# Kernel tuning notes

Measured on AMD Instinct MI355X. Metric: run time of the kernel, lower is better.

## Reference

```python
import jax, jax.numpy as jnp
import numpy as np

L, H, DK, DV, D, DH, V, S, B = 2, 12, 64, 64, 768, 3072, 32000, 1024, 2


def _layernorm(x):
    # matches custom LayerNorm: mean over last dim, biased std, no eps, no affine
    mu = jnp.mean(x, axis=-1, keepdims=True)
    sigma = jnp.sqrt(jnp.mean(jnp.square(x - mu), axis=-1, keepdims=True))
    return (x - mu) / sigma


def setup_inputs() -> dict:
    key = jax.random.key(0)
    ks = jax.random.split(key, 12)
    n = lambda k, shp: (0.02 * jax.random.normal(k, shp, dtype=jnp.float32))
    return {
        "x": jax.random.randint(ks[0], (B, S), 0, V),
        "ignore": jax.random.randint(ks[1], (B, S), 0, 2).astype(jnp.int32),
        "emb": n(ks[2], (V, D)),
        "pos": n(ks[3], (S, D)),
        "Wq": n(ks[4], (L, H, D, DK)), "bq": jnp.zeros((L, H, DK), jnp.float32),
        "Wk": n(ks[5], (L, H, D, DK)), "bk": jnp.zeros((L, H, DK), jnp.float32),
        "Wv": n(ks[6], (L, H, D, DV)), "bv": jnp.zeros((L, H, DV), jnp.float32),
        "Wo": n(ks[7], (L, H * DV, D)), "bo": jnp.zeros((L, D), jnp.float32),
        "W1": n(ks[8], (L, D, DH)), "b1": jnp.zeros((L, DH), jnp.float32),
        "W2": n(ks[9], (L, DH, D)), "b2": jnp.zeros((L, D), jnp.float32),
        "Wout": n(ks[10], (D, V)), "bout": jnp.zeros((V,), jnp.float32),
    }


def reference(x, ignore, emb, pos, Wq, bq, Wk, bk, Wv, bv, Wo, bo, W1, b1, W2, b2, Wout, bout):
    b, s = x.shape
    ign0 = (ignore == 0)  # True = valid token
    # token emb + position emb zeroed on ignored positions (dropout = eval/identity)
    h = emb[x] + pos[None, :, :] * ign0[:, :, None].astype(emb.dtype)

    # mask[b,i,j]: attend iff j<=i AND (ignore[j]==0 OR i==j)  (diagonal always kept)
    causal = jnp.tril(jnp.ones((s, s), dtype=bool))
    eye = jnp.eye(s, dtype=bool)
    allow = (ign0[:, None, None, :] | eye[None, None, :, :]) & causal[None, None, :, :]  # [b,1,i,j]

    scale = jnp.sqrt(jnp.asarray(DK, h.dtype))
    for l in range(L):
        q = jnp.einsum('bsd,hdk->bhsk', h, Wq[l]) + bq[l][None, :, None, :]
        k = jnp.einsum('bsd,hdk->bhsk', h, Wk[l]) + bk[l][None, :, None, :]
        v = jnp.einsum('bsd,hdv->bhsv', h, Wv[l]) + bv[l][None, :, None, :]
        scores = jnp.einsum('bhik,bhjk->bhij', q, k) / scale
        scores = jnp.where(allow, scores, -jnp.inf)
        p = jax.nn.softmax(scores, axis=-1)
        sa = jnp.einsum('bhij,bhjv->bhiv', p, v)
        sa = sa.transpose(0, 2, 1, 3).reshape(b, s, H * DV)  # concat heads (head-major order matches torch cat)
        attn_out = sa @ Wo[l] + bo[l]
        z = _layernorm(h + attn_out)
        # NOTE: original FeedForwardLayer applies GELU AFTER linear2 (faithful to source)
        f = jax.nn.gelu((z @ W1[l] + b1[l]) @ W2[l] + b2[l], approximate=False)
        h = _layernorm(z + f)
    return h @ Wout + bout
```

## Files before the change

kernel.cpp:

```cpp
#include <hip/hip_runtime.h>
#include <math.h>

static constexpr int L_ = 2, H_ = 12, D_ = 768, DH_ = 3072, V_ = 32000,
                     S_ = 1024, B_ = 2;
static constexpr int M_ = B_ * S_;

typedef __attribute__((ext_vector_type(4))) float f32x4;
typedef __attribute__((ext_vector_type(8))) short s16x8;
typedef __attribute__((ext_vector_type(2))) unsigned int u32x2;
typedef __attribute__((ext_vector_type(4))) unsigned int u32x4;

__device__ __forceinline__ unsigned short f2bf(float f) {
    unsigned u = __builtin_bit_cast(unsigned, f);
    u = (u + 0x7FFFu + ((u >> 16) & 1u)) >> 16;
    return (unsigned short)u;
}
__device__ __forceinline__ unsigned pack2(float a, float b) {
    return (unsigned)f2bf(a) | ((unsigned)f2bf(b) << 16);
}

__device__ __forceinline__ void gld16(const void* g, void* l) {
    __builtin_amdgcn_global_load_lds(
        (const __attribute__((address_space(1))) unsigned int*)g,
        (__attribute__((address_space(3))) unsigned int*)l, 16, 0, 0);
}

__global__ __launch_bounds__(256) void wtr_kernel(
    const float* __restrict__ in, unsigned short* __restrict__ out, int K, int N)
{
    __shared__ unsigned short t[64 * 68];
    const size_t mo = (size_t)blockIdx.z * K * N;
    in  += mo; out += mo;
    const int n0 = blockIdx.x * 64, k0 = blockIdx.y * 64;
    const int tid = threadIdx.x;
    const int kr = tid >> 2, nc = (tid & 3) * 16;
    const float* src = in + (size_t)(k0 + kr) * N + n0 + nc;
    #pragma unroll
    for (int j = 0; j < 4; ++j) {
        const float4 v = *(const float4*)(src + j * 4);
        *(u32x2*)&t[kr * 68 + nc + j * 4] = (u32x2){pack2(v.x, v.y), pack2(v.z, v.w)};
    }
    __syncthreads();
    const int nr = tid >> 2, kc = (tid & 3) * 16;
    unsigned short v16[16];
    #pragma unroll
    for (int j = 0; j < 16; ++j) v16[j] = t[(kc + j) * 68 + nr];
    unsigned short* dst = out + (size_t)(n0 + nr) * K + k0 + kc;
    ((u32x4*)dst)[0] = *(u32x4*)&v16[0];
    ((u32x4*)dst)[1] = *(u32x4*)&v16[8];
}

__global__ __launch_bounds__(256) void wtr3_kernel(
    const float* __restrict__ Wq, const float* __restrict__ Wk,
    const float* __restrict__ Wv, unsigned short* __restrict__ oq,
    unsigned short* __restrict__ ok, unsigned short* __restrict__ ov)
{
    __shared__ unsigned short t[64 * 68];
    const int z = blockIdx.z;
    const int which = z / 24, zz = z - which * 24;
    const float* in = (which == 0) ? Wq : (which == 1) ? Wk : Wv;
    unsigned short* out = (which == 0) ? oq : (which == 1) ? ok : ov;
    const size_t mo = (size_t)zz * D_ * 64;
    in += mo; out += mo;
    const int k0 = blockIdx.y * 64;
    const int tid = threadIdx.x;
    const int kr = tid >> 2, nc = (tid & 3) * 16;
    const float* src = in + (size_t)(k0 + kr) * 64 + nc;
    #pragma unroll
    for (int j = 0; j < 4; ++j) {
        const float4 v = *(const float4*)(src + j * 4);
        *(u32x2*)&t[kr * 68 + nc + j * 4] = (u32x2){pack2(v.x, v.y), pack2(v.z, v.w)};
    }
    __syncthreads();
    const int nr = tid >> 2, kc = (tid & 3) * 16;
    unsigned short v16[16];
    #pragma unroll
    for (int j = 0; j < 16; ++j) v16[j] = t[(kc + j) * 68 + nr];
    unsigned short* dst = out + (size_t)nr * D_ + k0 + kc;
    ((u32x4*)dst)[0] = *(u32x4*)&v16[0];
    ((u32x4*)dst)[1] = *(u32x4*)&v16[8];
}

__device__ __forceinline__ void gemm_bt_body(
    const unsigned short* __restrict__ A, const unsigned short* __restrict__ BT,
    const float* __restrict__ bias, void* __restrict__ Cp,
    int N, int K, int act, int bx, int by)
{
    __shared__ unsigned short AB[16384];
    unsigned short* As = AB;
    unsigned short* Bs = AB + 8192;
    const int tid = threadIdx.x;
    const int l   = tid & 63, wid = tid >> 6;
    const int wr  = wid >> 1, wc = wid & 1;
    const int brow = by * 128, bn = bx * 128;

    f32x4 acc[4][4];
    #pragma unroll
    for (int i = 0; i < 4; ++i)
        #pragma unroll
        for (int j = 0; j < 4; ++j) acc[i][j] = (f32x4)0.f;

    const int arow = tid >> 3;
    const int aq   = (tid & 7) ^ (arow & 7);
    const unsigned short* Abase = A  + (size_t)(brow + arow) * K + aq * 8;
    const unsigned short* Bbase = BT + (size_t)(bn   + arow) * K + aq * 8;

    for (int k0 = 0; k0 < K; k0 += 64) {
        #pragma unroll
        for (int r = 0; r < 4; ++r)
            gld16(Abase + (size_t)r * 32 * K + k0, (char*)As + r * 4096 + wid * 1024);
        #pragma unroll
        for (int r = 0; r < 4; ++r)
            gld16(Bbase + (size_t)r * 32 * K + k0, (char*)Bs + r * 4096 + wid * 1024);
        __syncthreads();

        #pragma unroll
        for (int kk = 0; kk < 2; ++kk) {
            s16x8 af[4], bf[4];
            #pragma unroll
            for (int mf = 0; mf < 4; ++mf) {
                const int row = wr * 64 + mf * 16 + (l & 15);
                const int gg  = (kk * 4 + (l >> 4)) ^ (row & 7);
                af[mf] = *(const s16x8*)((const char*)As + row * 128 + gg * 16);
            }
            #pragma unroll
            for (int nf = 0; nf < 4; ++nf) {
                const int col = wc * 64 + nf * 16 + (l & 15);
                const int gg  = (kk * 4 + (l >> 4)) ^ (col & 7);
                bf[nf] = *(const s16x8*)((const char*)Bs + col * 128 + gg * 16);
            }
            #pragma unroll
            for (int mf = 0; mf < 4; ++mf)
                #pragma unroll
                for (int nf = 0; nf < 4; ++nf)
                    acc[mf][nf] = __builtin_amdgcn_mfma_f32_16x16x32_bf16(
                        af[mf], bf[nf], acc[mf][nf], 0, 0, 0);
        }
        __syncthreads();
    }

    const int lr = l >> 4, lc = l & 15;
    if (act == 3) {
        #pragma unroll
        for (int nf = 0; nf < 4; ++nf) {
            const int c = wc * 64 + nf * 16 + lc;
            const float bb = bias[bn + c];
            #pragma unroll
            for (int mf = 0; mf < 4; ++mf) {
                const int srel = wr * 64 + mf * 16 + lr * 4;
                u32x2 pk;
                pk[0] = pack2(acc[mf][nf][0] + bb, acc[mf][nf][1] + bb);
                pk[1] = pack2(acc[mf][nf][2] + bb, acc[mf][nf][3] + bb);
                const int byo = (c * 256 + srel * 2) ^ ((c & 7) << 4);
                *(u32x2*)((char*)AB + byo) = pk;
            }
        }
        __syncthreads();
        const int row = tid >> 1, half = tid & 1;
        const int gcf = bn + row;
        const int head = gcf >> 6, d = gcf & 63;
        const int b = brow >> 10;
        const int sb = (brow & (S_ - 1)) + half * 64;
        unsigned short* dst = (unsigned short*)Cp +
            (((size_t)b * H_ + head) * 64 + d) * S_ + sb;
        #pragma unroll
        for (int u = 0; u < 8; ++u) {
            const int byo = (row * 256 + half * 128 + u * 16) ^ ((row & 7) << 4);
            ((u32x4*)dst)[u] = *(const u32x4*)((const char*)AB + byo);
        }
        return;
    }
    #pragma unroll
    for (int nf = 0; nf < 4; ++nf) {
        const int gcol = bn + wc * 64 + nf * 16 + lc;
        const float bb = bias[gcol];
        #pragma unroll
        for (int mf = 0; mf < 4; ++mf) {
            #pragma unroll
            for (int rg = 0; rg < 4; ++rg) {
                const int grow = brow + wr * 64 + mf * 16 + lr * 4 + rg;
                float vv = acc[mf][nf][rg] + bb;
                if (act == 1) vv = 0.5f * vv * (1.0f + erff(vv * 0.70710678118654752f));
                if (act == 2)
                    ((unsigned short*)Cp)[(size_t)grow * N + gcol] = f2bf(vv);
                else
                    ((float*)Cp)[(size_t)grow * N + gcol] = vv;
            }
        }
    }
}

__device__ __forceinline__ void xcd_decode(int& bx, int& by) {
    const int gx = gridDim.x, gy = gridDim.y;
    const int nwg = gx * gy;
    const int flat = blockIdx.y * gx + blockIdx.x;
    const int s = (flat & 7) * (nwg >> 3) + (flat >> 3);
    bx = s / gy;
    by = s % gy;
}

__global__ __launch_bounds__(256) void gemm_bt(
    const unsigned short* __restrict__ A, const unsigned short* __restrict__ BT,
    const float* __restrict__ bias, void* __restrict__ C, int N, int K, int act)
{
    int bx, by; xcd_decode(bx, by);
    gemm_bt_body(A, BT, bias, C, N, K, act, bx, by);
}

__global__ __launch_bounds__(256) void gemm_qkv3(
    const unsigned short* __restrict__ A,
    const unsigned short* __restrict__ qT, const unsigned short* __restrict__ kT,
    const unsigned short* __restrict__ vT,
    const float* __restrict__ bq, const float* __restrict__ bk, const float* __restrict__ bv,
    unsigned short* __restrict__ q, unsigned short* __restrict__ k,
    unsigned short* __restrict__ v)
{
    const unsigned short* BT; const float* bi; unsigned short* C; int act;
    if (blockIdx.z == 0)      { BT = qT; bi = bq; C = q; act = 2; }
    else if (blockIdx.z == 1) { BT = kT; bi = bk; C = k; act = 2; }
    else                      { BT = vT; bi = bv; C = v; act = 3; }
    int bx, by; xcd_decode(bx, by);
    gemm_bt_body(A, BT, bi, C, 768, 768, act, bx, by);
}

__global__ __launch_bounds__(256) void gemm_bt64(
    const unsigned short* __restrict__ A, const unsigned short* __restrict__ BT,
    const float* __restrict__ bias, float* __restrict__ C, int N, int K, int act)
{
    __shared__ unsigned short As[4096];
    __shared__ unsigned short Bs[8192];
    const int tid = threadIdx.x;
    const int l = tid & 63, w = tid >> 6;
    const int lq = l & 15, lg = l >> 4;
    int bx, by; xcd_decode(bx, by);
    const int brow = by * 64, bn = bx * 128;

    f32x4 acc[4][2];
    #pragma unroll
    for (int i = 0; i < 4; ++i)
        #pragma unroll
        for (int j = 0; j < 2; ++j) acc[i][j] = (f32x4)0.f;

    const int arow = tid >> 3;
    const int aq   = (tid & 7) ^ (arow & 7);
    const unsigned short* Abase = A  + (size_t)(brow + arow) * K + aq * 8;
    const unsigned short* Bbase = BT + (size_t)(bn   + arow) * K + aq * 8;

    for (int k0 = 0; k0 < K; k0 += 64) {
        #pragma unroll
        for (int r = 0; r < 2; ++r)
            gld16(Abase + (size_t)r * 32 * K + k0, (char*)As + r * 4096 + tid * 16);
        #pragma unroll
        for (int r = 0; r < 4; ++r)
            gld16(Bbase + (size_t)r * 32 * K + k0, (char*)Bs + r * 4096 + tid * 16);
        __syncthreads();

        #pragma unroll
        for (int kk = 0; kk < 2; ++kk) {
            s16x8 af[4], bf[2];
            #pragma unroll
            for (int mf = 0; mf < 4; ++mf) {
                const int row = mf * 16 + lq;
                const int gg  = (kk * 4 + lg) ^ (row & 7);
                af[mf] = *(const s16x8*)((const char*)As + row * 128 + gg * 16);
            }
            #pragma unroll
            for (int nf = 0; nf < 2; ++nf) {
                const int col = w * 32 + nf * 16 + lq;
                const int gg  = (kk * 4 + lg) ^ (col & 7);
                bf[nf] = *(const s16x8*)((const char*)Bs + col * 128 + gg * 16);
            }
            #pragma unroll
            for (int mf = 0; mf < 4; ++mf)
                #pragma unroll
                for (int nf = 0; nf < 2; ++nf)
                    acc[mf][nf] = __builtin_amdgcn_mfma_f32_16x16x32_bf16(
                        af[mf], bf[nf], acc[mf][nf], 0, 0, 0);
        }
        __syncthreads();
    }

    #pragma unroll
    for (int nf = 0; nf < 2; ++nf) {
        const int gcol = bn + w * 32 + nf * 16 + lq;
        const float bb = bias[gcol];
        #pragma unroll
        for (int mf = 0; mf < 4; ++mf)
            #pragma unroll
            for (int rg = 0; rg < 4; ++rg) {
                const int grow = brow + mf * 16 + lg * 4 + rg;
                float vv = acc[mf][nf][rg] + bb;
                if (act == 1) vv = 0.5f * vv * (1.0f + erff(vv * 0.70710678118654752f));
                C[(size_t)grow * N + gcol] = vv;
            }
    }
}

__global__ __launch_bounds__(512, 2) void gemm_deep(
    const unsigned short* __restrict__ A, const unsigned short* __restrict__ BT,
    const float* __restrict__ bias, float* __restrict__ C, int N, int K)
{
    __shared__ char lds[131072];
    const int tid = threadIdx.x;
    const int l = tid & 63, w = tid >> 6;
    const int wr = w >> 2, wc = w & 3;
    const int lq = l & 15, lg = l >> 4;

    int bx, by;
    {
        const int gx = gridDim.x, gy = gridDim.y;
        const int nwg = gx * gy;
        const int flat = blockIdx.y * gx + blockIdx.x;
        const int s = (flat & 7) * (nwg >> 3) + (flat >> 3);
        bx = s / gy; by = s % gy;
    }
    const int brow = by * 256, bn = bx * 256;
    const int NT = K >> 6;

    const int srow = (w << 3) + (l >> 3);
    const int sgr  = (l & 7) ^ (l >> 3);
    const size_t soff = (size_t)srow * K + sgr * 8;
    const unsigned short* Ag = A  + (size_t)brow * K + soff;
    const unsigned short* Bg = BT + (size_t)bn   * K + soff;
    const size_t r64  = (size_t)64 * K;
    const size_t r128 = (size_t)128 * K;
    char* const dA = lds + w * 1024;
    char* const dB = lds + 65536 + w * 1024;

#define STG_A(CB, HF, KT) do {                                                   \
    gld16(Ag + (size_t)(HF) * r128 + (size_t)(KT) * 64,                          \
          dA + (CB) * 32768 + (HF) * 16384);                                     \
    gld16(Ag + (size_t)(HF) * r128 + r64 + (size_t)(KT) * 64,                    \
          dA + (CB) * 32768 + (HF) * 16384 + 8192); } while (0)
#define STG_B(CB, HF, KT) do {                                                   \
    gld16(Bg + (size_t)(HF) * r128 + (size_t)(KT) * 64,                          \
          dB + (CB) * 32768 + (HF) * 16384);                                     \
    gld16(Bg + (size_t)(HF) * r128 + r64 + (size_t)(KT) * 64,                    \
          dB + (CB) * 32768 + (HF) * 16384 + 8192); } while (0)

    f32x4 acc[8][4];
    #pragma unroll
    for (int i = 0; i < 8; ++i)
        #pragma unroll
        for (int j = 0; j < 4; ++j) acc[i][j] = (f32x4)0.f;

    STG_A(0, 0, 0); STG_A(0, 1, 0); STG_B(0, 0, 0); STG_B(0, 1, 0);
    STG_A(1, 0, 1); STG_B(1, 0, 1);
    asm volatile("s_waitcnt vmcnt(4)" ::: "memory");
    __builtin_amdgcn_s_barrier();

    for (int t = 0; t < NT; ++t) {
        const int c = t & 1;
        const char* Ab = lds + c * 32768;
        const char* Bb = lds + 65536 + c * 32768;
        s16x8 af[4], bf[4];

        #pragma unroll
        for (int mf = 0; mf < 4; ++mf) {
            const int row = wr * 128 + mf * 16 + lq;
            af[mf] = *(const s16x8*)(Ab + row * 128 + ((lg ^ (row & 7)) << 4));
        }
        #pragma unroll
        for (int nf = 0; nf < 4; ++nf) {
            const int col = wc * 64 + nf * 16 + lq;
            bf[nf] = *(const s16x8*)(Bb + col * 128 + ((lg ^ (col & 7)) << 4));
        }
        if (t + 1 < NT) STG_A(c ^ 1, 1, t + 1);
        asm volatile("s_waitcnt lgkmcnt(0)" ::: "memory");
        __builtin_amdgcn_sched_barrier(0);
        __builtin_amdgcn_s_barrier();
        __builtin_amdgcn_s_setprio(1);
        #pragma unroll
        for (int mf = 0; mf < 4; ++mf)
            #pragma unroll
            for (int nf = 0; nf < 4; ++nf)
                acc[mf][nf] = __builtin_amdgcn_mfma_f32_16x16x32_bf16(
                    af[mf], bf[nf], acc[mf][nf], 0, 0, 0);
        __builtin_amdgcn_s_setprio(0);
        __builtin_amdgcn_s_barrier();

        #pragma unroll
        for (int mf = 0; mf < 4; ++mf) {
            const int row = wr * 128 + (mf + 4) * 16 + lq;
            af[mf] = *(const s16x8*)(Ab + row * 128 + ((lg ^ (row & 7)) << 4));
        }
        if (t + 1 < NT) STG_B(c ^ 1, 1, t + 1);
        asm volatile("s_waitcnt lgkmcnt(0)" ::: "memory");
        __builtin_amdgcn_sched_barrier(0);
        __builtin_amdgcn_s_barrier();
        __builtin_amdgcn_s_setprio(1);
        #pragma unroll
        for (int mf = 0; mf < 4; ++mf)
            #pragma unroll
            for (int nf = 0; nf < 4; ++nf)
                acc[mf + 4][nf] = __builtin_amdgcn_mfma_f32_16x16x32_bf16(
                    af[mf], bf[nf], acc[mf + 4][nf], 0, 0, 0);
        __builtin_amdgcn_s_setprio(0);
        __builtin_amdgcn_s_barrier();

        #pragma unroll
        for (int mf = 0; mf < 4; ++mf) {
            const int row = wr * 128 + mf * 16 + lq;
            af[mf] = *(const s16x8*)(Ab + row * 128 + (((4 + lg) ^ (row & 7)) << 4));
        }
        #pragma unroll
        for (int nf = 0; nf < 4; ++nf) {
            const int col = wc * 64 + nf * 16 + lq;
            bf[nf] = *(const s16x8*)(Bb + col * 128 + (((4 + lg) ^ (col & 7)) << 4));
        }
        asm volatile("s_waitcnt lgkmcnt(0)" ::: "memory");
        __builtin_amdgcn_sched_barrier(0);
        __builtin_amdgcn_s_barrier();
        __builtin_amdgcn_s_setprio(1);
        #pragma unroll
        for (int mf = 0; mf < 4; ++mf)
            #pragma unroll
            for (int nf = 0; nf < 4; ++nf)
                acc[mf][nf] = __builtin_amdgcn_mfma_f32_16x16x32_bf16(
                    af[mf], bf[nf], acc[mf][nf], 0, 0, 0);
        __builtin_amdgcn_s_setprio(0);
        __builtin_amdgcn_s_barrier();

        #pragma unroll
        for (int mf = 0; mf < 4; ++mf) {
            const int row = wr * 128 + (mf + 4) * 16 + lq;
            af[mf] = *(const s16x8*)(Ab + row * 128 + (((4 + lg) ^ (row & 7)) << 4));
        }
        asm volatile("s_waitcnt lgkmcnt(0)" ::: "memory");
        __builtin_amdgcn_sched_barrier(0);
        __builtin_amdgcn_s_barrier();
        __builtin_amdgcn_s_setprio(1);
        #pragma unroll
        for (int mf = 0; mf < 4; ++mf)
            #pragma unroll
            for (int nf = 0; nf < 4; ++nf)
                acc[mf + 4][nf] = __builtin_amdgcn_mfma_f32_16x16x32_bf16(
                    af[mf], bf[nf], acc[mf + 4][nf], 0, 0, 0);
        __builtin_amdgcn_s_setprio(0);

        if (t + 2 < NT) {
            STG_A(c, 0, t + 2); STG_B(c, 0, t + 2);
            asm volatile("s_waitcnt vmcnt(4)" ::: "memory");
            __builtin_amdgcn_s_barrier();
        } else if (t + 1 < NT) {
            asm volatile("s_waitcnt vmcnt(0)" ::: "memory");
            __builtin_amdgcn_s_barrier();
        }
    }
#undef STG_A
#undef STG_B

    #pragma unroll
    for (int nf = 0; nf < 4; ++nf) {
        const int gcol = bn + wc * 64 + nf * 16 + lq;
        const float bb = bias[gcol];
        #pragma unroll
        for (int mf = 0; mf < 8; ++mf)
            #pragma unroll
            for (int rg = 0; rg < 4; ++rg) {
                const int grow = brow + wr * 128 + mf * 16 + lg * 4 + rg;
                C[(size_t)grow * N + gcol] = acc[mf][nf][rg] + bb;
            }
    }
}

__global__ __launch_bounds__(256) void gemm_f32b(
    const unsigned short* __restrict__ A, const float* __restrict__ B,
    const float* __restrict__ bias, float* __restrict__ C, int N, int K)
{
    __shared__ unsigned short As[8192];
    __shared__ unsigned short Bs[8192];
    const int tid = threadIdx.x;
    const int l   = tid & 63, wid = tid >> 6;
    const int wr  = wid >> 1, wc = wid & 1;
    const int brow = blockIdx.y * 128, bn = blockIdx.x * 128;
    f32x4 acc[4][4];
    #pragma unroll
    for (int i = 0; i < 4; ++i)
        #pragma unroll
        for (int j = 0; j < 4; ++j) acc[i][j] = (f32x4)0.f;
    const int arow = tid >> 3;
    const int aq   = (tid & 7) ^ (arow & 7);
    const int bkq  = tid >> 5, bnq = tid & 31;
    for (int k0 = 0; k0 < K; k0 += 64) {
        #pragma unroll
        for (int r = 0; r < 4; ++r)
            gld16(A + (size_t)(brow + r * 32 + arow) * K + k0 + aq * 8,
                  (char*)As + r * 4096 + wid * 1024);
        #pragma unroll
        for (int r = 0; r < 2; ++r) {
            const int kb = r * 32 + bkq * 4;
            const float* pp = B + (size_t)(k0 + kb) * N + bn + bnq * 4;
            const float4 v0 = *(const float4*)(pp);
            const float4 v1 = *(const float4*)(pp + N);
            const float4 v2 = *(const float4*)(pp + 2 * (size_t)N);
            const float4 v3 = *(const float4*)(pp + 3 * (size_t)N);
            const int g = kb >> 3, bytek = (kb & 4) * 2;
            const float* f0 = (const float*)&v0; const float* f1 = (const float*)&v1;
            const float* f2 = (const float*)&v2; const float* f3 = (const float*)&v3;
            #pragma unroll
            for (int i = 0; i < 4; ++i) {
                const int n = bnq * 4 + i;
                char* dst = (char*)Bs + n * 128 + ((g ^ (n & 7)) * 16) + bytek;
                *(u32x2*)dst = (u32x2){pack2(f0[i], f1[i]), pack2(f2[i], f3[i])};
            }
        }
        __syncthreads();
        #pragma unroll
        for (int kk = 0; kk < 2; ++kk) {
            s16x8 af[4], bf[4];
            #pragma unroll
            for (int mf = 0; mf < 4; ++mf) {
                const int row = wr * 64 + mf * 16 + (l & 15);
                const int gg  = (kk * 4 + (l >> 4)) ^ (row & 7);
                af[mf] = *(const s16x8*)((const char*)As + row * 128 + gg * 16);
            }
            #pragma unroll
            for (int nf = 0; nf < 4; ++nf) {
                const int col = wc * 64 + nf * 16 + (l & 15);
                const int gg  = (kk * 4 + (l >> 4)) ^ (col & 7);
                bf[nf] = *(const s16x8*)((const char*)Bs + col * 128 + gg * 16);
            }
            #pragma unroll
            for (int mf = 0; mf < 4; ++mf)
                #pragma unroll
                for (int nf = 0; nf < 4; ++nf)
                    acc[mf][nf] = __builtin_amdgcn_mfma_f32_16x16x32_bf16(
                        af[mf], bf[nf], acc[mf][nf], 0, 0, 0);
        }
        __syncthreads();
    }
    const int lr = l >> 4, lc = l & 15;
    #pragma unroll
    for (int nf = 0; nf < 4; ++nf) {
        const int gcol = bn + wc * 64 + nf * 16 + lc;
        const float bb = bias[gcol];
        #pragma unroll
        for (int mf = 0; mf < 4; ++mf)
            #pragma unroll
            for (int rg = 0; rg < 4; ++rg) {
                const int grow = brow + wr * 64 + mf * 16 + lr * 4 + rg;
                C[(size_t)grow * N + gcol] = acc[mf][nf][rg] + bb;
            }
    }
}

__global__ __launch_bounds__(256) void fattn_kernel(
    const unsigned short* __restrict__ qm, const unsigned short* __restrict__ km,
    const unsigned short* __restrict__ vt, const int* __restrict__ ign,
    unsigned short* __restrict__ sab)
{
    __shared__ unsigned short Ks[2][4096];
    __shared__ unsigned short VTs[2][4096];
    __shared__ float addvs[2][64];
    __shared__ unsigned short PTs[4][1024];

    const int hh = blockIdx.y, b = blockIdx.z;
    const int zy = b * 12 + hh;
    const int qt = (zy >= 16) ? (15 - blockIdx.x) : blockIdx.x;

    const int tid = threadIdx.x;
    const int l = tid & 63, w = tid >> 6;
    const int g = l >> 4, lq = l & 15;
    const int i = qt * 64 + w * 16 + lq;

    const size_t qgb = ((size_t)(b * S_ + i)) * D_ + hh * 64;
    const s16x8 qf0 = *(const s16x8*)(qm + qgb + g * 8);
    const s16x8 qf1 = *(const s16x8*)(qm + qgb + 32 + g * 8);

    f32x4 accO[4];
    #pragma unroll
    for (int d = 0; d < 4; ++d) accO[d] = (f32x4)0.f;
    float mrun = -1e30f, lrun = 0.f;

    const int srow = tid >> 3, sg = tid & 7;
    const size_t kbase = (size_t)(b * S_) * D_ + hh * 64;
    const size_t vbase = ((size_t)(b * H_ + hh) * 64) * S_;

    auto stage = [&](int t, int bufi) {
        const int j0 = t * 64;
        #pragma unroll
        for (int r = 0; r < 2; ++r) {
            const int row = r * 32 + srow;
            const int gsw = (sg ^ (row & 7)) * 8;
            gld16(km + kbase + (size_t)(j0 + row) * D_ + gsw,
                  (char*)&Ks[bufi][0] + (r * 256 + tid) * 16);
            gld16(vt + vbase + (size_t)row * S_ + j0 + gsw,
                  (char*)&VTs[bufi][0] + (r * 256 + tid) * 16);
        }
        if (tid < 64)
            addvs[bufi][tid] = (ign[b * S_ + j0 + tid] == 0) ? 0.f : -INFINITY;
    };

    stage(0, 0);
    asm volatile("s_waitcnt vmcnt(0) lgkmcnt(0)" ::: "memory");
    __syncthreads();

    for (int t = 0; t <= qt; ++t) {
        const int cur = t & 1;
        const int j0 = t * 64;
        if (t < qt) stage(t + 1, cur ^ 1);

        f32x4 adv[4];
        #pragma unroll
        for (int kf = 0; kf < 4; ++kf)
            adv[kf] = *(const f32x4*)&addvs[cur][kf * 16 + g * 4];

        f32x4 sacc[4];
        #pragma unroll
        for (int kf = 0; kf < 4; ++kf) sacc[kf] = (f32x4)0.f;
        __builtin_amdgcn_s_setprio(1);
        #pragma unroll
        for (int kk = 0; kk < 2; ++kk) {
            const s16x8 qv = kk ? qf1 : qf0;
            #pragma unroll
            for (int kf = 0; kf < 4; ++kf) {
                const int row = kf * 16 + lq;
                const s16x8 kv = *(const s16x8*)((const char*)&Ks[cur][0] + row * 128 +
                                                 (((kk * 4 + g) ^ (row & 7)) * 16));
                sacc[kf] = __builtin_amdgcn_mfma_f32_16x16x32_bf16(kv, qv, sacc[kf], 0, 0, 0);
            }
        }
        __builtin_amdgcn_s_setprio(0);

        float tmax = -INFINITY;
        if (t < qt) {
            #pragma unroll
            for (int kf = 0; kf < 4; ++kf)
                #pragma unroll
                for (int rg = 0; rg < 4; ++rg) {
                    const float s = fmaf(sacc[kf][rg], 0.125f, adv[kf][rg]);
                    sacc[kf][rg] = s;
                    tmax = fmaxf(tmax, s);
                }
        } else {
            #pragma unroll
            for (int kf = 0; kf < 4; ++kf)
                #pragma unroll
                for (int rg = 0; rg < 4; ++rg) {
                    const int j = j0 + kf * 16 + g * 4 + rg;
                    const float sv = sacc[kf][rg] * 0.125f;
                    const float s = (j > i) ? -INFINITY
                                  : (j == i ? sv : sv + adv[kf][rg]);
                    sacc[kf][rg] = s;
                    tmax = fmaxf(tmax, s);
                }
        }
        tmax = fmaxf(tmax, __shfl_xor(tmax, 16));
        tmax = fmaxf(tmax, __shfl_xor(tmax, 32));
        const float mnew = fmaxf(mrun, tmax);
        const float fac = __expf(mrun - mnew);
        float psum = 0.f;
        #pragma unroll
        for (int kf = 0; kf < 4; ++kf)
            #pragma unroll
            for (int rg = 0; rg < 4; ++rg) {
                const float p = __expf(sacc[kf][rg] - mnew);
                sacc[kf][rg] = p;
                psum += p;
            }
        psum += __shfl_xor(psum, 16);
        psum += __shfl_xor(psum, 32);
        lrun = lrun * fac + psum;
        mrun = mnew;
        #pragma unroll
        for (int d = 0; d < 4; ++d) accO[d] *= fac;

        char* ptw = (char*)&PTs[w][0];
        #pragma unroll
        for (int kf = 0; kf < 4; ++kf) {
            u32x2 pk;
            pk[0] = pack2(sacc[kf][0], sacc[kf][1]);
            pk[1] = pack2(sacc[kf][2], sacc[kf][3]);
            *(u32x2*)(ptw + lq * 128 +
                      (((kf * 2 + (g >> 1)) ^ (lq & 7)) * 16) + (g & 1) * 8) = pk;
        }
        __builtin_amdgcn_s_setprio(1);
        #pragma unroll
        for (int kh = 0; kh < 2; ++kh) {
            const s16x8 pb = *(const s16x8*)(ptw + lq * 128 +
                                             (((kh * 4 + g) ^ (lq & 7)) * 16));
            #pragma unroll
            for (int df = 0; df < 4; ++df) {
                const int row = df * 16 + lq;
                const s16x8 vf = *(const s16x8*)((const char*)&VTs[cur][0] + row * 128 +
                                                 (((kh * 4 + g) ^ (row & 7)) * 16));
                accO[df] = __builtin_amdgcn_mfma_f32_16x16x32_bf16(vf, pb, accO[df], 0, 0, 0);
            }
        }
        __builtin_amdgcn_s_setprio(0);
        asm volatile("s_waitcnt vmcnt(0)" ::: "memory");
        __syncthreads();
    }

    const float inv = 1.0f / lrun;
    unsigned short* orow = sab + ((size_t)(b * S_ + i)) * D_ + hh * 64;
    #pragma unroll
    for (int df = 0; df < 4; ++df) {
        u32x2 pk;
        pk[0] = pack2(accO[df][0] * inv, accO[df][1] * inv);
        pk[1] = pack2(accO[df][2] * inv, accO[df][3] * inv);
        *(u32x2*)(orow + df * 16 + g * 4) = pk;
    }
}

__global__ __launch_bounds__(256) void embed_kernel(
    const int* __restrict__ x, const int* __restrict__ ign,
    const float* __restrict__ emb, const float* __restrict__ pos,
    float* __restrict__ h, unsigned short* __restrict__ hbf)
{
    const int row = blockIdx.x;
    const int s = row & (S_ - 1);
    const int tok = x[row];
    const float keep = (ign[row] == 0) ? 1.0f : 0.0f;
    const float* er = emb + (size_t)tok * D_;
    const float* pr = pos + (size_t)s * D_;
    float* hr = h + (size_t)row * D_;
    unsigned short* hb = hbf + (size_t)row * D_;
    for (int d = threadIdx.x; d < D_; d += 256) {
        const float t = er[d] + pr[d] * keep;
        hr[d] = t;
        hb[d] = f2bf(t);
    }
}

__global__ __launch_bounds__(256) void add_ln_kernel(
    const float* __restrict__ X, const float* __restrict__ Y,
    float* __restrict__ out, unsigned short* __restrict__ outbf)
{
    const int row = blockIdx.x * 4 + (threadIdx.x >> 6);
    const int l = threadIdx.x & 63;
    const float4* xr = (const float4*)(X + (size_t)row * D_);
    const float4* yr = (const float4*)(Y + (size_t)row * D_);
    float4 t[3];
    float s0 = 0.f;
    #pragma unroll
    for (int k = 0; k < 3; ++k) {
        const float4 a = xr[k * 64 + l], b = yr[k * 64 + l];
        t[k].x = a.x + b.x; t[k].y = a.y + b.y;
        t[k].z = a.z + b.z; t[k].w = a.w + b.w;
        s0 += t[k].x + t[k].y + t[k].z + t[k].w;
    }
    #pragma unroll
    for (int o = 32; o; o >>= 1) s0 += __shfl_xor(s0, o);
    const float mu = s0 * (1.0f / D_);
    float s1 = 0.f;
    #pragma unroll
    for (int k = 0; k < 3; ++k) {
        t[k].x -= mu; t[k].y -= mu; t[k].z -= mu; t[k].w -= mu;
        s1 += t[k].x * t[k].x + t[k].y * t[k].y + t[k].z * t[k].z + t[k].w * t[k].w;
    }
    #pragma unroll
    for (int o = 32; o; o >>= 1) s1 += __shfl_xor(s1, o);
    const float inv = 1.0f / sqrtf(s1 * (1.0f / D_));
    float4* orow = (float4*)(out + (size_t)row * D_);
    u32x2* obf = (u32x2*)(outbf + (size_t)row * D_);
    #pragma unroll
    for (int k = 0; k < 3; ++k) {
        float4 r;
        r.x = t[k].x * inv; r.y = t[k].y * inv;
        r.z = t[k].z * inv; r.w = t[k].w * inv;
        orow[k * 64 + l] = r;
        u32x2 pk; pk[0] = pack2(r.x, r.y); pk[1] = pack2(r.z, r.w);
        obf[k * 64 + l] = pk;
    }
}

extern "C" void kernel_launch(void* const* d_in, const int* in_sizes, int n_in,
                              void* d_out, int out_size, void* d_ws, size_t ws_size,
                              hipStream_t stream)
{
    const int*   x    = (const int*)d_in[0];
    const int*   ign  = (const int*)d_in[1];
    const float* emb  = (const float*)d_in[2];
    const float* pos  = (const float*)d_in[3];
    const float* Wq   = (const float*)d_in[4];
    const float* bq   = (const float*)d_in[5];
    const float* Wk   = (const float*)d_in[6];
    const float* bk   = (const float*)d_in[7];
    const float* Wv   = (const float*)d_in[8];
    const float* bv   = (const float*)d_in[9];
    const float* Wo   = (const float*)d_in[10];
    const float* bo   = (const float*)d_in[11];
    const float* W1   = (const float*)d_in[12];
    const float* b1   = (const float*)d_in[13];
    const float* W2   = (const float*)d_in[14];
    const float* b2   = (const float*)d_in[15];
    const float* Wout = (const float*)d_in[16];
    const float* bout = (const float*)d_in[17];
    float* outp = (float*)d_out;

    const size_t RC = (size_t)M_ * D_;
    const size_t F1 = (size_t)M_ * DH_;
    const size_t WH = (size_t)H_ * 64 * D_;
    const size_t WF = (size_t)D_ * DH_;
    const size_t WOUTE = (size_t)V_ * D_;

    char* wsp = (char*)d_ws;
    size_t wsleft = ws_size;
    char* dop = (char*)d_out;
    auto alloc = [&](size_t bytes, bool must_ws) -> void* {
        bytes = (bytes + 255) & ~(size_t)255;
        if (wsleft >= bytes) { void* p = wsp; wsp += bytes; wsleft -= bytes; return p; }
        if (must_ws) return nullptr;
        void* p = dop; dop += bytes; return p;
    };

    unsigned short* hbf   = (unsigned short*)alloc(RC * 2, true);
    unsigned short* woutT = (unsigned short*)alloc(WOUTE * 2, true);
    float* h   = (float*)alloc(RC * 4, false);
    float* z   = (float*)alloc(RC * 4, false);
    float* tmp = (float*)alloc(RC * 4, false);
    unsigned short* zbf   = (unsigned short*)alloc(RC * 2, false);
    unsigned short* sabbf = (unsigned short*)alloc(RC * 2, false);
    unsigned short* qbf   = (unsigned short*)alloc(RC * 2, false);
    unsigned short* kbf   = (unsigned short*)alloc(RC * 2, false);
    unsigned short* vtb   = (unsigned short*)alloc(RC * 2, false);
    unsigned short* f1bf  = (unsigned short*)alloc(F1 * 2, false);
    unsigned short* wqT = (unsigned short*)alloc(L_ * WH * 2, false);
    unsigned short* wkT = (unsigned short*)alloc(L_ * WH * 2, false);
    unsigned short* wvT = (unsigned short*)alloc(L_ * WH * 2, false);
    unsigned short* woT = (unsigned short*)alloc(L_ * WH * 2, false);
    unsigned short* w1T = (unsigned short*)alloc(L_ * WF * 2, false);
    unsigned short* w2T = (unsigned short*)alloc(L_ * WF * 2, false);

    embed_kernel<<<M_, 256, 0, stream>>>(x, ign, emb, pos, h, hbf);

    wtr3_kernel<<<dim3(1, 12, 72), 256, 0, stream>>>(Wq, Wk, Wv, wqT, wkT, wvT);
    wtr_kernel<<<dim3(12, 12, L_), 256, 0, stream>>>(Wo, woT, D_, D_);
    wtr_kernel<<<dim3(48, 12, L_), 256, 0, stream>>>(W1, w1T, D_, DH_);
    wtr_kernel<<<dim3(12, 48, L_), 256, 0, stream>>>(W2, w2T, DH_, D_);
    if (woutT)
        wtr_kernel<<<dim3(V_ / 64, 12, 1), 256, 0, stream>>>(Wout, woutT, D_, V_);

    for (int l = 0; l < L_; ++l) {
        gemm_qkv3<<<dim3(6, 16, 3), 256, 0, stream>>>(
            hbf, wqT + l * WH, wkT + l * WH, wvT + l * WH,
            bq + l * 768, bk + l * 768, bv + l * 768, qbf, kbf, vtb);

        fattn_kernel<<<dim3(S_ / 64, H_, B_), 256, 0, stream>>>(
            qbf, kbf, vtb, ign, sabbf);

        gemm_bt64<<<dim3(6, 32), 256, 0, stream>>>(
            sabbf, woT + l * WH, bo + l * D_, tmp, D_, D_, 0);
        add_ln_kernel<<<M_ / 4, 256, 0, stream>>>(h, tmp, z, zbf);

        gemm_bt<<<dim3(24, 16), 256, 0, stream>>>(
            zbf, w1T + l * WF, b1 + l * DH_, f1bf, DH_, D_, 2);
        gemm_bt64<<<dim3(6, 32), 256, 0, stream>>>(
            f1bf, w2T + l * WF, b2 + l * D_, tmp, D_, DH_, 1);
        add_ln_kernel<<<M_ / 4, 256, 0, stream>>>(z, tmp, h, hbf);
    }

    if (woutT)
        gemm_deep<<<dim3(V_ / 256, M_ / 256), 512, 0, stream>>>(
            hbf, woutT, bout, outp, V_, D_);
    else
        gemm_f32b<<<dim3(V_ / 128, M_ / 128), 256, 0, stream>>>(
            hbf, Wout, bout, outp, V_, D_);
}
```

Before: 536.3 us.

## Use 64-row tiles for QKV/W1 GEMMs and split-K the W2 GEMM

Replaces the 128x128 tile GEMM with a shared 64x128 tile body for the QKV and W1 projections, doubling the block count to fill more CUs. The W2 GEMM (K=3072) is split into two K halves written to separate buffers, and the GELU plus partial-sum reduction moves into the add+layernorm kernel. This removes a wave-quantization and low-parallelism cost, at the price of an extra fp32 buffer read/write and more A-tile reloads. The launch bounds on gemm_deep also drop the min-blocks hint.

```diff
diff --git a/kernel.cpp b/kernel.cpp
--- a/kernel.cpp
+++ b/kernel.cpp
@@ -81,115 +81,6 @@
     ((u32x4*)dst)[1] = *(u32x4*)&v16[8];
 }
 
-__device__ __forceinline__ void gemm_bt_body(
-    const unsigned short* __restrict__ A, const unsigned short* __restrict__ BT,
-    const float* __restrict__ bias, void* __restrict__ Cp,
-    int N, int K, int act, int bx, int by)
-{
-    __shared__ unsigned short AB[16384];
-    unsigned short* As = AB;
-    unsigned short* Bs = AB + 8192;
-    const int tid = threadIdx.x;
-    const int l   = tid & 63, wid = tid >> 6;
-    const int wr  = wid >> 1, wc = wid & 1;
-    const int brow = by * 128, bn = bx * 128;
-
-    f32x4 acc[4][4];
-    #pragma unroll
-    for (int i = 0; i < 4; ++i)
-        #pragma unroll
-        for (int j = 0; j < 4; ++j) acc[i][j] = (f32x4)0.f;
-
-    const int arow = tid >> 3;
-    const int aq   = (tid & 7) ^ (arow & 7);
-    const unsigned short* Abase = A  + (size_t)(brow + arow) * K + aq * 8;
-    const unsigned short* Bbase = BT + (size_t)(bn   + arow) * K + aq * 8;
-
-    for (int k0 = 0; k0 < K; k0 += 64) {
-        #pragma unroll
-        for (int r = 0; r < 4; ++r)
-            gld16(Abase + (size_t)r * 32 * K + k0, (char*)As + r * 4096 + wid * 1024);
-        #pragma unroll
-        for (int r = 0; r < 4; ++r)
-            gld16(Bbase + (size_t)r * 32 * K + k0, (char*)Bs + r * 4096 + wid * 1024);
-        __syncthreads();
-
-        #pragma unroll
-        for (int kk = 0; kk < 2; ++kk) {
-            s16x8 af[4], bf[4];
-            #pragma unroll
-            for (int mf = 0; mf < 4; ++mf) {
-                const int row = wr * 64 + mf * 16 + (l & 15);
-                const int gg  = (kk * 4 + (l >> 4)) ^ (row & 7);
-                af[mf] = *(const s16x8*)((const char*)As + row * 128 + gg * 16);
-            }
-            #pragma unroll
-            for (int nf = 0; nf < 4; ++nf) {
-                const int col = wc * 64 + nf * 16 + (l & 15);
-                const int gg  = (kk * 4 + (l >> 4)) ^ (col & 7);
-                bf[nf] = *(const s16x8*)((const char*)Bs + col * 128 + gg * 16);
-            }
-            #pragma unroll
-            for (int mf = 0; mf < 4; ++mf)
-                #pragma unroll
-                for (int nf = 0; nf < 4; ++nf)
-                    acc[mf][nf] = __builtin_amdgcn_mfma_f32_16x16x32_bf16(
-                        af[mf], bf[nf], acc[mf][nf], 0, 0, 0);
-        }
-        __syncthreads();
-    }
-
-    const int lr = l >> 4, lc = l & 15;
-    if (act == 3) {
-        #pragma unroll
-        for (int nf = 0; nf < 4; ++nf) {
-            const int c = wc * 64 + nf * 16 + lc;
-            const float bb = bias[bn + c];
-            #pragma unroll
-            for (int mf = 0; mf < 4; ++mf) {
-                const int srel = wr * 64 + mf * 16 + lr * 4;
-                u32x2 pk;
-                pk[0] = pack2(acc[mf][nf][0] + bb, acc[mf][nf][1] + bb);
-                pk[1] = pack2(acc[mf][nf][2] + bb, acc[mf][nf][3] + bb);
-                const int byo = (c * 256 + srel * 2) ^ ((c & 7) << 4);
-                *(u32x2*)((char*)AB + byo) = pk;
-            }
-        }
-        __syncthreads();
-        const int row = tid >> 1, half = tid & 1;
-        const int gcf = bn + row;
-        const int head = gcf >> 6, d = gcf & 63;
-        const int b = brow >> 10;
-        const int sb = (brow & (S_ - 1)) + half * 64;
-        unsigned short* dst = (unsigned short*)Cp +
-            (((size_t)b * H_ + head) * 64 + d) * S_ + sb;
-        #pragma unroll
-        for (int u = 0; u < 8; ++u) {
-            const int byo = (row * 256 + half * 128 + u * 16) ^ ((row & 7) << 4);
-            ((u32x4*)dst)[u] = *(const u32x4*)((const char*)AB + byo);
-        }
-        return;
-    }
-    #pragma unroll
-    for (int nf = 0; nf < 4; ++nf) {
-        const int gcol = bn + wc * 64 + nf * 16 + lc;
-        const float bb = bias[gcol];
-        #pragma unroll
-        for (int mf = 0; mf < 4; ++mf) {
-            #pragma unroll
-            for (int rg = 0; rg < 4; ++rg) {
-                const int grow = brow + wr * 64 + mf * 16 + lr * 4 + rg;
-                float vv = acc[mf][nf][rg] + bb;
-                if (act == 1) vv = 0.5f * vv * (1.0f + erff(vv * 0.70710678118654752f));
-                if (act == 2)
-                    ((unsigned short*)Cp)[(size_t)grow * N + gcol] = f2bf(vv);
-                else
-                    ((float*)Cp)[(size_t)grow * N + gcol] = vv;
-            }
-        }
-    }
-}
-
 __device__ __forceinline__ void xcd_decode(int& bx, int& by) {
     const int gx = gridDim.x, gy = gridDim.y;
     const int nwg = gx * gy;
@@ -199,15 +90,122 @@
     by = s % gy;
 }
 
-__global__ __launch_bounds__(256) void gemm_bt(
+__device__ __forceinline__ void bt64_body(
+    const unsigned short* __restrict__ A, const unsigned short* __restrict__ BT,
+    const float* __restrict__ bias, void* __restrict__ Cp,
+    int N, int K, int act, int k0off, int klen, int bx, int by)
+{
+    __shared__ unsigned short AB[12288];
+    unsigned short* As = AB;
+    unsigned short* Bs = AB + 4096;
+    const int tid = threadIdx.x;
+    const int l = tid & 63, w = tid >> 6;
+    const int lq = l & 15, lg = l >> 4;
+    const int brow = by * 64, bn = bx * 128;
+
+    f32x4 acc[4][2];
+    #pragma unroll
+    for (int i = 0; i < 4; ++i)
+        #pragma unroll
+        for (int j = 0; j < 2; ++j) acc[i][j] = (f32x4)0.f;
+
+    const int arow = tid >> 3;
+    const int aq   = (tid & 7) ^ (arow & 7);
+    const unsigned short* Abase = A  + (size_t)(brow + arow) * K + k0off + aq * 8;
+    const unsigned short* Bbase = BT + (size_t)(bn   + arow) * K + k0off + aq * 8;
+
+    for (int k0 = 0; k0 < klen; k0 += 64) {
+        #pragma unroll
+        for (int r = 0; r < 2; ++r)
+            gld16(Abase + (size_t)r * 32 * K + k0, (char*)As + r * 4096 + tid * 16);
+        #pragma unroll
+        for (int r = 0; r < 4; ++r)
+            gld16(Bbase + (size_t)r * 32 * K + k0, (char*)Bs + r * 4096 + tid * 16);
+        __syncthreads();
+
+        #pragma unroll
+        for (int kk = 0; kk < 2; ++kk) {
+            s16x8 af[4], bf[2];
+            #pragma unroll
+            for (int mf = 0; mf < 4; ++mf) {
+                const int row = mf * 16 + lq;
+                const int gg  = (kk * 4 + lg) ^ (row & 7);
+                af[mf] = *(const s16x8*)((const char*)As + row * 128 + gg * 16);
+            }
+            #pragma unroll
+            for (int nf = 0; nf < 2; ++nf) {
+                const int col = w * 32 + nf * 16 + lq;
+                const int gg  = (kk * 4 + lg) ^ (col & 7);
+                bf[nf] = *(const s16x8*)((const char*)Bs + col * 128 + gg * 16);
+            }
+            #pragma unroll
+            for (int mf = 0; mf < 4; ++mf)
+                #pragma unroll
+                for (int nf = 0; nf < 2; ++nf)
+                    acc[mf][nf] = __builtin_amdgcn_mfma_f32_16x16x32_bf16(
+                        af[mf], bf[nf], acc[mf][nf], 0, 0, 0);
+        }
+        __syncthreads();
+    }
+
+    if (act == 3) {
+        #pragma unroll
+        for (int nf = 0; nf < 2; ++nf) {
+            const int c = w * 32 + nf * 16 + lq;
+            const float bb = bias[bn + c];
+            #pragma unroll
+            for (int mf = 0; mf < 4; ++mf) {
+                const int srel = mf * 16 + lg * 4;
+                u32x2 pk;
+                pk[0] = pack2(acc[mf][nf][0] + bb, acc[mf][nf][1] + bb);
+                pk[1] = pack2(acc[mf][nf][2] + bb, acc[mf][nf][3] + bb);
+                const int byo = (c * 128 + srel * 2) ^ ((c & 7) << 4);
+                *(u32x2*)((char*)AB + byo) = pk;
+            }
+        }
+        __syncthreads();
+        const int row = tid >> 1, half = tid & 1;
+        const int gcf = bn + row;
+        const int head = gcf >> 6, d = gcf & 63;
+        const int b = brow >> 10;
+        const int sb = (brow & (S_ - 1)) + half * 32;
+        unsigned short* dst = (unsigned short*)Cp +
+            (((size_t)b * H_ + head) * 64 + d) * S_ + sb;
+        #pragma unroll
+        for (int u = 0; u < 4; ++u) {
+            const int byo = (row * 128 + half * 64 + u * 16) ^ ((row & 7) << 4);
+            ((u32x4*)dst)[u] = *(const u32x4*)((const char*)AB + byo);
+        }
+        return;
+    }
+    #pragma unroll
+    for (int nf = 0; nf < 2; ++nf) {
+        const int gcol = bn + w * 32 + nf * 16 + lq;
+        const float bb = (act == 4) ? 0.f : bias[gcol];
+        #pragma unroll
+        for (int mf = 0; mf < 4; ++mf)
+            #pragma unroll
+            for (int rg = 0; rg < 4; ++rg) {
+                const int grow = brow + mf * 16 + lg * 4 + rg;
+                float vv = acc[mf][nf][rg] + bb;
+                if (act == 1) vv = 0.5f * vv * (1.0f + erff(vv * 0.70710678118654752f));
+                if (act == 2)
+                    ((unsigned short*)Cp)[(size_t)grow * N + gcol] = f2bf(vv);
+                else
+                    ((float*)Cp)[(size_t)grow * N + gcol] = vv;
+            }
+    }
+}
+
+__global__ __launch_bounds__(256) void gemm_bt64(
     const unsigned short* __restrict__ A, const unsigned short* __restrict__ BT,
     const float* __restrict__ bias, void* __restrict__ C, int N, int K, int act)
 {
     int bx, by; xcd_decode(bx, by);
-    gemm_bt_body(A, BT, bias, C, N, K, act, bx, by);
-}
-
-__global__ __launch_bounds__(256) void gemm_qkv3(
+    bt64_body(A, BT, bias, C, N, K, act, 0, K, bx, by);
+}
+
+__global__ __launch_bounds__(256) void gemm_qkv64(
     const unsigned short* __restrict__ A,
     const unsigned short* __restrict__ qT, const unsigned short* __restrict__ kT,
     const unsigned short* __restrict__ vT,
@@ -220,83 +218,21 @@
     else if (blockIdx.z == 1) { BT = kT; bi = bk; C = k; act = 2; }
     else                      { BT = vT; bi = bv; C = v; act = 3; }
     int bx, by; xcd_decode(bx, by);
-    gemm_bt_body(A, BT, bi, C, 768, 768, act, bx, by);
-}
-
-__global__ __launch_bounds__(256) void gemm_bt64(
+    bt64_body(A, BT, bi, C, 768, 768, act, 0, 768, bx, by);
+}
+
+__global__ __launch_bounds__(256) void gemm_w2sk(
     const unsigned short* __restrict__ A, const unsigned short* __restrict__ BT,
-    const float* __restrict__ bias, float* __restrict__ C, int N, int K, int act)
-{
-    __shared__ unsigned short As[4096];
-    __shared__ unsigned short Bs[8192];
-    const int tid = threadIdx.x;
-    const int l = tid & 63, w = tid >> 6;
-    const int lq = l & 15, lg = l >> 4;
+    const float* __restrict__ bias, float* __restrict__ C0, float* __restrict__ C1)
+{
     int bx, by; xcd_decode(bx, by);
-    const int brow = by * 64, bn = bx * 128;
-
-    f32x4 acc[4][2];
-    #pragma unroll
-    for (int i = 0; i < 4; ++i)
-        #pragma unroll
-        for (int j = 0; j < 2; ++j) acc[i][j] = (f32x4)0.f;
-
-    const int arow = tid >> 3;
-    const int aq   = (tid & 7) ^ (arow & 7);
-    const unsigned short* Abase = A  + (size_t)(brow + arow) * K + aq * 8;
-    const unsigned short* Bbase = BT + (size_t)(bn   + arow) * K + aq * 8;
-
-    for (int k0 = 0; k0 < K; k0 += 64) {
-        #pragma unroll
-        for (int r = 0; r < 2; ++r)
-            gld16(Abase + (size_t)r * 32 * K + k0, (char*)As + r * 4096 + tid * 16);
-        #pragma unroll
-        for (int r = 0; r < 4; ++r)
-            gld16(Bbase + (size_t)r * 32 * K + k0, (char*)Bs + r * 4096 + tid * 16);
-        __syncthreads();
-
-        #pragma unroll
-        for (int kk = 0; kk < 2; ++kk) {
-            s16x8 af[4], bf[2];
-            #pragma unroll
-            for (int mf = 0; mf < 4; ++mf) {
-                const int row = mf * 16 + lq;
-                const int gg  = (kk * 4 + lg) ^ (row & 7);
-                af[mf] = *(const s16x8*)((const char*)As + row * 128 + gg * 16);
-            }
-            #pragma unroll
-            for (int nf = 0; nf < 2; ++nf) {
-                const int col = w * 32 + nf * 16 + lq;
-                const int gg  = (kk * 4 + lg) ^ (col & 7);
-                bf[nf] = *(const s16x8*)((const char*)Bs + col * 128 + gg * 16);
-            }
-            #pragma unroll
-            for (int mf = 0; mf < 4; ++mf)
-                #pragma unroll
-                for (int nf = 0; nf < 2; ++nf)
-                    acc[mf][nf] = __builtin_amdgcn_mfma_f32_16x16x32_bf16(
-                        af[mf], bf[nf], acc[mf][nf], 0, 0, 0);
-        }
-        __syncthreads();
-    }
-
-    #pragma unroll
-    for (int nf = 0; nf < 2; ++nf) {
-        const int gcol = bn + w * 32 + nf * 16 + lq;
-        const float bb = bias[gcol];
-        #pragma unroll
-        for (int mf = 0; mf < 4; ++mf)
-            #pragma unroll
-            for (int rg = 0; rg < 4; ++rg) {
-                const int grow = brow + mf * 16 + lg * 4 + rg;
-                float vv = acc[mf][nf][rg] + bb;
-                if (act == 1) vv = 0.5f * vv * (1.0f + erff(vv * 0.70710678118654752f));
-                C[(size_t)grow * N + gcol] = vv;
-            }
-    }
-}
-
-__global__ __launch_bounds__(512, 2) void gemm_deep(
+    if (blockIdx.z == 0)
+        bt64_body(A, BT, bias, C0, 768, DH_, 0, 0, 1536, bx, by);
+    else
+        bt64_body(A, BT, bias, C1, 768, DH_, 4, 1536, 1536, bx, by);
+}
+
+__global__ __launch_bounds__(512) void gemm_deep(
     const unsigned short* __restrict__ A, const unsigned short* __restrict__ BT,
     const float* __restrict__ bias, float* __restrict__ C, int N, int K)
 {
@@ -725,18 +661,29 @@
 }
 
 __global__ __launch_bounds__(256) void add_ln_kernel(
-    const float* __restrict__ X, const float* __restrict__ Y,
-    float* __restrict__ out, unsigned short* __restrict__ outbf)
+    const float* __restrict__ X, const float* __restrict__ Y0,
+    const float* __restrict__ Y1, float* __restrict__ out,
+    unsigned short* __restrict__ outbf, int mode)
 {
     const int row = blockIdx.x * 4 + (threadIdx.x >> 6);
     const int l = threadIdx.x & 63;
     const float4* xr = (const float4*)(X + (size_t)row * D_);
-    const float4* yr = (const float4*)(Y + (size_t)row * D_);
+    const float4* y0 = (const float4*)(Y0 + (size_t)row * D_);
+    const float4* y1 = (const float4*)(Y1 + (size_t)row * D_);
     float4 t[3];
     float s0 = 0.f;
     #pragma unroll
     for (int k = 0; k < 3; ++k) {
-        const float4 a = xr[k * 64 + l], b = yr[k * 64 + l];
+        const float4 a = xr[k * 64 + l];
+        float4 b = y0[k * 64 + l];
+        if (mode == 1) {
+            const float4 c = y1[k * 64 + l];
+            b.x += c.x; b.y += c.y; b.z += c.z; b.w += c.w;
+            b.x = 0.5f * b.x * (1.0f + erff(b.x * 0.70710678118654752f));
+            b.y = 0.5f * b.y * (1.0f + erff(b.y * 0.70710678118654752f));
+            b.z = 0.5f * b.z * (1.0f + erff(b.z * 0.70710678118654752f));
+            b.w = 0.5f * b.w * (1.0f + erff(b.w * 0.70710678118654752f));
+        }
         t[k].x = a.x + b.x; t[k].y = a.y + b.y;
         t[k].z = a.z + b.z; t[k].w = a.w + b.w;
         s0 += t[k].x + t[k].y + t[k].z + t[k].w;
@@ -808,9 +755,10 @@
 
     unsigned short* hbf   = (unsigned short*)alloc(RC * 2, true);
     unsigned short* woutT = (unsigned short*)alloc(WOUTE * 2, true);
-    float* h   = (float*)alloc(RC * 4, false);
-    float* z   = (float*)alloc(RC * 4, false);
-    float* tmp = (float*)alloc(RC * 4, false);
+    float* h    = (float*)alloc(RC * 4, false);
+    float* z    = (float*)alloc(RC * 4, false);
+    float* tmp  = (float*)alloc(RC * 4, false);
+    float* tmp1 = (float*)alloc(RC * 4, false);
     unsigned short* zbf   = (unsigned short*)alloc(RC * 2, false);
     unsigned short* sabbf = (unsigned short*)alloc(RC * 2, false);
     unsigned short* qbf   = (unsigned short*)alloc(RC * 2, false);
@@ -834,7 +782,7 @@
         wtr_kernel<<<dim3(V_ / 64, 12, 1), 256, 0, stream>>>(Wout, woutT, D_, V_);
 
     for (int l = 0; l < L_; ++l) {
-        gemm_qkv3<<<dim3(6, 16, 3), 256, 0, stream>>>(
+        gemm_qkv64<<<dim3(6, 32, 3), 256, 0, stream>>>(
             hbf, wqT + l * WH, wkT + l * WH, wvT + l * WH,
             bq + l * 768, bk + l * 768, bv + l * 768, qbf, kbf, vtb);
 
@@ -843,13 +791,13 @@
 
         gemm_bt64<<<dim3(6, 32), 256, 0, stream>>>(
             sabbf, woT + l * WH, bo + l * D_, tmp, D_, D_, 0);
-        add_ln_kernel<<<M_ / 4, 256, 0, stream>>>(h, tmp, z, zbf);
-
-        gemm_bt<<<dim3(24, 16), 256, 0, stream>>>(
+        add_ln_kernel<<<M_ / 4, 256, 0, stream>>>(h, tmp, tmp, z, zbf, 0);
+
+        gemm_bt64<<<dim3(24, 32), 256, 0, stream>>>(
             zbf, w1T + l * WF, b1 + l * DH_, f1bf, DH_, D_, 2);
-        gemm_bt64<<<dim3(6, 32), 256, 0, stream>>>(
-            f1bf, w2T + l * WF, b2 + l * D_, tmp, D_, DH_, 1);
-        add_ln_kernel<<<M_ / 4, 256, 0, stream>>>(z, tmp, h, hbf);
+        gemm_w2sk<<<dim3(6, 32, 2), 256, 0, stream>>>(
+            f1bf, w2T + l * WF, b2 + l * D_, tmp, tmp1);
+        add_ln_kernel<<<M_ / 4, 256, 0, stream>>>(z, tmp, tmp1, h, hbf, 1);
     }
 
     if (woutT)
```

New measurement: 451.4 us. -15.8%, faster.
